# Kernel tuning notes

Measured on AMD Instinct MI355X. Metric: run time of the kernel, lower is better.

## Reference

```python
import jax, jax.numpy as jnp
import numpy as np

DEPTH = 6
N_EST = 16
IN_DIM = 512
N_CLASSES = 100
BATCH = 8192
N_NODES = 2 ** DEPTH - 1   # 63 internal nodes
N_LEAVES = 2 ** DEPTH      # 64 leaves


def entmax15(t):
    # Source's (nonstandard) entmax15: softmax(relu(t)**1.5)
    z = jax.nn.relu(t)
    return jax.nn.softmax(z ** 1.5, axis=-1)


def _leaf_paths():
    # Ancestor node index and branch bit for every (depth level j, leaf l),
    # exactly matching: idx = 2**(j-1) + l // 2**(depth-(j-1)) - 1
    #                   bit = (l // 2**(depth-j)) % 2
    l = np.arange(N_LEAVES)
    j = np.arange(1, DEPTH + 1)[:, None]
    idx = (2 ** (j - 1) + l[None, :] // (2 ** (DEPTH - (j - 1))) - 1).astype(np.int32)
    bits = ((l[None, :] // (2 ** (DEPTH - j))) % 2).astype(np.int32)
    return jnp.asarray(idx), jnp.asarray(bits)  # both (DEPTH, N_LEAVES)


def setup_inputs() -> dict:
    key = jax.random.key(0)
    kx, kT, kL = jax.random.split(key, 3)
    x = jax.random.normal(kx, (BATCH, IN_DIM), dtype=jnp.float32)
    T = jax.random.normal(kT, (N_EST, N_NODES, IN_DIM), dtype=jnp.float32)
    L = jax.random.normal(kL, (N_EST, N_LEAVES, N_CLASSES), dtype=jnp.float32)
    return {"x": x, "T": T, "L": L}


def reference(x, T, L):
    # Hard feature selection with straight-through: forward = hardmax(entmax15(T)),
    # backward = 0 (in the torch source, I = I - (I - hardmax(I)) kills the gradient).
    I_soft = entmax15(T)  # (E, N, D)
    I = jax.lax.stop_gradient(
        (I_soft == I_soft.max(axis=-1, keepdims=True)).astype(x.dtype)
    )
    # Per-node split decisions for all nodes at once.
    t_dot = jnp.einsum('end,end->en', T, I)          # (E, N) threshold value
    x_dot = jnp.einsum('bd,end->ben', x, I)          # (B, E, N) selected feature
    # s = s - (s - floor(s)) == floor(s); floor has zero gradient (matches torch).
    s = jnp.floor(t_dot[None, :, :] - x_dot)         # (B, E, N)

    idx, bits = _leaf_paths()                        # (DEPTH, N_LEAVES)
    sg = s[..., idx]                                 # (B, E, DEPTH, N_LEAVES)
    factors = jnp.where(bits[None, None] == 1, 1.0 - sg, sg)
    p = jnp.prod(factors, axis=2)                    # (B, E, N_LEAVES)

    # Leaf values, summed over the ensemble.
    y_hat = jnp.einsum('bel,elc->bc', p, L)          # (B, C)
    return jax.nn.softmax(y_hat, axis=-1)
```

## Files before the change

### kernel.cpp

```cpp
#include <hip/hip_runtime.h>
#include <hip/hip_bf16.h>
#include <math.h>

#define IN_DIM 512
#define NC 100
#define NN 63
#define NE 16
#define BATCH 8192
#define XP 516
#define RP 132

typedef __attribute__((ext_vector_type(8))) short bf16x8;
typedef __attribute__((ext_vector_type(4))) float f32x4;

static __device__ __forceinline__ ushort bf16_bits(__hip_bfloat16 h) {
  union { __hip_bfloat16 b; ushort u; } cv; cv.b = h; return cv.u;
}

__global__ __launch_bounds__(256) void prep_kernel(
    const float* __restrict__ T, const float* __restrict__ L,
    ushort* __restrict__ Bfrag, float* __restrict__ tmax, int* __restrict__ dstar) {
  const int tid = threadIdx.x;
  const int bid = blockIdx.x;

  {
    const int i = bid * 256 + tid;
    const int j = i & 7;
    const int lane = (i >> 3) & 63;
    const int cf = (i >> 9) & 7;
    const int hl = (i >> 12) & 1;
    const int kc = i >> 13;
    const int k = kc * 32 + (lane >> 4) * 8 + j;
    const int c = cf * 16 + (lane & 15);
    const float val = (c < NC) ? L[(size_t)k * NC + c] : 0.0f;
    const __hip_bfloat16 hb = __float2bfloat16(val);
    ushort outv;
    if (hl == 0) {
      outv = bf16_bits(hb);
    } else {
      const __hip_bfloat16 lb = __float2bfloat16(val - __bfloat162float(hb));
      outv = bf16_bits(lb);
    }
    Bfrag[i] = outv;
  }

  if (bid < NE * NN && tid < 64) {
    const float4* row = reinterpret_cast<const float4*>(T + (size_t)bid * IN_DIM);
    const int lane = tid;
    float best = -INFINITY;
    int bidx = 0;
#pragma unroll
    for (int i = 0; i < 2; ++i) {
      const int f4 = lane + 64 * i;
      const float4 v = row[f4];
      const int base = f4 * 4;
      if (v.x > best) { best = v.x; bidx = base; }
      if (v.y > best) { best = v.y; bidx = base + 1; }
      if (v.z > best) { best = v.z; bidx = base + 2; }
      if (v.w > best) { best = v.w; bidx = base + 3; }
    }
#pragma unroll
    for (int off = 32; off; off >>= 1) {
      const float ov = __shfl_xor(best, off);
      const int oi = __shfl_xor(bidx, off);
      if (ov > best || (ov == best && oi < bidx)) { best = ov; bidx = oi; }
    }
    if (lane == 0) {
      tmax[bid] = best;
      dstar[bid] = bidx;
    }
  }
}

__global__ __launch_bounds__(512, 2) void forest_fused_kernel(
    const float* __restrict__ x, const ushort* __restrict__ Bfrag,
    const float* __restrict__ tmaxg, const int* __restrict__ dstarg,
    float* __restrict__ out) {
  __shared__ __align__(16) float xl[32 * XP];
  __shared__ __align__(16) int2 tds[NE * 64];
  __shared__ __align__(16) float red[8 * 16 * RP];
  const int tid = threadIdx.x;
  const int b0 = blockIdx.x * 32;
  const int w = tid >> 6, lane = tid & 63;

  {
    const float4* xg = reinterpret_cast<const float4*>(x + (size_t)b0 * IN_DIM);
#pragma unroll
    for (int i = 0; i < 8; ++i) {
      const int idx = tid + i * 512;
      const int r = idx >> 7, c4 = idx & 127;
      *reinterpret_cast<float4*>(&xl[r * XP + c4 * 4]) = xg[r * 128 + c4];
    }
    for (int i = tid; i < NE * NN; i += 512) {
      const int e = (i * 1041) >> 16;
      const int n = i - e * 63;
      tds[e * 64 + 1 + n] = make_int2(dstarg[i], __float_as_int(tmaxg[i]));
    }
  }
  __syncthreads();

  const int r = lane & 15;
  const int lgq = lane >> 4;
  const float* xr0 = &xl[r * XP];
  const float* xr1 = &xl[(r + 16) * XP];
  const bf16x8* bf = reinterpret_cast<const bf16x8*>(Bfrag);

  f32x4 acc0[8], acc1[8];
#pragma unroll
  for (int cf = 0; cf < 8; ++cf) { acc0[cf] = (f32x4)0.0f; acc1[cf] = (f32x4)0.0f; }

  for (int t = 0; t < 4; ++t) {
    const int kc = w * 4 + t;
    const int e = kc >> 1;
    const int lg = (kc & 1) * 4 + lgq;

    const size_t bbase = (size_t)kc * 1024;
    bf16x8 BH[8], BL[8];
#pragma unroll
    for (int cf = 0; cf < 8; ++cf) {
      BH[cf] = bf[bbase + (size_t)cf * 64 + lane];
      BL[cf] = bf[bbase + 512 + (size_t)cf * 64 + lane];
    }

    const int2* tb = &tds[e * 64];
    const int2 T1 = tb[1];
    const int2 T2 = tb[2 + (lg >> 2)];
    const int2 T3 = tb[4 + (lg >> 1)];
    const int2 T4 = tb[8 + lg];
    const int4 P5 = *reinterpret_cast<const int4*>(&tb[16 + 2 * lg]);
    const int4 Q0 = *reinterpret_cast<const int4*>(&tb[32 + 4 * lg]);
    const int4 Q1 = *reinterpret_cast<const int4*>(&tb[34 + 4 * lg]);

    bf16x8 Ah, Al;
    auto agen = [&](const float* xr) {
      const float s1 = floorf(__int_as_float(T1.y) - xr[T1.x]);
      const float s2 = floorf(__int_as_float(T2.y) - xr[T2.x]);
      const float s3 = floorf(__int_as_float(T3.y) - xr[T3.x]);
      const float s4 = floorf(__int_as_float(T4.y) - xr[T4.x]);
      const float s5a = floorf(__int_as_float(P5.y) - xr[P5.x]);
      const float s5b = floorf(__int_as_float(P5.w) - xr[P5.z]);
      const float s60 = floorf(__int_as_float(Q0.y) - xr[Q0.x]);
      const float s61 = floorf(__int_as_float(Q0.w) - xr[Q0.z]);
      const float s62 = floorf(__int_as_float(Q1.y) - xr[Q1.x]);
      const float s63 = floorf(__int_as_float(Q1.w) - xr[Q1.z]);
      const float f1 = ((lg >> 2) & 1) ? 1.0f - s1 : s1;
      const float f2 = ((lg >> 1) & 1) ? 1.0f - s2 : s2;
      const float f3 = (lg & 1) ? 1.0f - s3 : s3;
      const float stem = f1 * f2 * f3;
      const float qa = stem * s4, qb = stem * (1.0f - s4);
      const float w00 = qa * s5a, w01 = qa * (1.0f - s5a);
      const float w10 = qb * s5b, w11 = qb * (1.0f - s5b);
      float p[8];
      p[0] = w00 * s60; p[1] = w00 * (1.0f - s60);
      p[2] = w01 * s61; p[3] = w01 * (1.0f - s61);
      p[4] = w10 * s62; p[5] = w10 * (1.0f - s62);
      p[6] = w11 * s63; p[7] = w11 * (1.0f - s63);
      union { ushort u[8]; bf16x8 v; } H, Lo;
#pragma unroll
      for (int i2 = 0; i2 < 8; ++i2) {
        const __hip_bfloat16 hb = __float2bfloat16(p[i2]);
        const float hf = __bfloat162float(hb);
        H.u[i2] = bf16_bits(hb);
        Lo.u[i2] = bf16_bits(__float2bfloat16(p[i2] - hf));
      }
      Ah = H.v; Al = Lo.v;
    };

    agen(xr0);
#pragma unroll
    for (int cf = 0; cf < 8; ++cf) {
      acc0[cf] = __builtin_amdgcn_mfma_f32_16x16x32_bf16(Ah, BH[cf], acc0[cf], 0, 0, 0);
      acc0[cf] = __builtin_amdgcn_mfma_f32_16x16x32_bf16(Al, BH[cf], acc0[cf], 0, 0, 0);
      acc0[cf] = __builtin_amdgcn_mfma_f32_16x16x32_bf16(Ah, BL[cf], acc0[cf], 0, 0, 0);
      acc0[cf] = __builtin_amdgcn_mfma_f32_16x16x32_bf16(Al, BL[cf], acc0[cf], 0, 0, 0);
    }
    agen(xr1);
#pragma unroll
    for (int cf = 0; cf < 8; ++cf) {
      acc1[cf] = __builtin_amdgcn_mfma_f32_16x16x32_bf16(Ah, BH[cf], acc1[cf], 0, 0, 0);
      acc1[cf] = __builtin_amdgcn_mfma_f32_16x16x32_bf16(Al, BH[cf], acc1[cf], 0, 0, 0);
      acc1[cf] = __builtin_amdgcn_mfma_f32_16x16x32_bf16(Ah, BL[cf], acc1[cf], 0, 0, 0);
      acc1[cf] = __builtin_amdgcn_mfma_f32_16x16x32_bf16(Al, BL[cf], acc1[cf], 0, 0, 0);
    }
  }

  const int rlo = (lane >> 4) * 4;
  const int cl = lane & 15;
  const int rr = tid >> 5;
  const int cg = tid & 31;

  auto epi = [&](const f32x4 (&ac)[8], int rowbase) {
#pragma unroll
    for (int cf = 0; cf < 8; ++cf)
#pragma unroll
      for (int jj = 0; jj < 4; ++jj)
        red[(w * 16 + rlo + jj) * RP + cf * 16 + cl] = ac[cf][jj];
    __syncthreads();
    float v[4] = {0.0f, 0.0f, 0.0f, 0.0f};
#pragma unroll
    for (int pw = 0; pw < 8; ++pw) {
      const float4 rv =
          *reinterpret_cast<const float4*>(&red[(pw * 16 + rr) * RP + cg * 4]);
      v[0] += rv.x; v[1] += rv.y; v[2] += rv.z; v[3] += rv.w;
    }
    float m = -INFINITY;
#pragma unroll
    for (int j = 0; j < 4; ++j)
      if (cg * 4 + j < NC) m = fmaxf(m, v[j]);
#pragma unroll
    for (int off = 1; off < 32; off <<= 1) m = fmaxf(m, __shfl_xor(m, off));
    float ev[4];
    float ss = 0.0f;
#pragma unroll
    for (int j = 0; j < 4; ++j) {
      ev[j] = (cg * 4 + j < NC) ? __expf(v[j] - m) : 0.0f;
      ss += ev[j];
    }
#pragma unroll
    for (int off = 1; off < 32; off <<= 1) ss += __shfl_xor(ss, off);
    const float inv = 1.0f / ss;
    if (cg < 25) {
      float* orow = out + (size_t)(b0 + rowbase + rr) * NC + cg * 4;
      *reinterpret_cast<float4*>(orow) =
          make_float4(ev[0] * inv, ev[1] * inv, ev[2] * inv, ev[3] * inv);
    }
  };

  epi(acc0, 0);
  __syncthreads();
  epi(acc1, 16);
}

extern "C" void kernel_launch(void* const* d_in, const int* in_sizes, int n_in,
                              void* d_out, int out_size, void* d_ws, size_t ws_size,
                              hipStream_t stream) {
  const float* x = (const float*)d_in[0];
  const float* T = (const float*)d_in[1];
  const float* L = (const float*)d_in[2];
  float* out = (float*)d_out;

  char* ws = (char*)d_ws;
  ushort* Bfrag = (ushort*)ws;
  float* tmax = (float*)(ws + 524288);
  int* dstar = (int*)(ws + 528384);

  prep_kernel<<<1024, 256, 0, stream>>>(T, L, Bfrag, tmax, dstar);
  forest_fused_kernel<<<BATCH / 32, 512, 0, stream>>>(x, Bfrag, tmax, dstar, out);
}
```

Baseline: 22.75 us.

## Halve rows per block to 16 and raise occupancy with smaller LDS footprint

Each block now handles 16 batch rows instead of 32, with one accumulator set instead of two. This halves the x tile and reduction buffer in LDS and allows launch bounds of 4 blocks per CU, giving twice as many blocks to spread over the CUs. The epilogue reduces the 8-wave partial sums in two column chunks through a narrower shared buffer, then does a single softmax per row. The cost is that every block must reload the full B fragment set, which doubles that global/L2 traffic for the same batch, and the per-block setup is repeated over more blocks.

New measurement: 24.31 us. 1.07x slower.

```diff
diff --git a/kernel.cpp b/kernel.cpp
--- a/kernel.cpp
+++ b/kernel.cpp
@@ -8,7 +8,7 @@
 #define NE 16
 #define BATCH 8192
 #define XP 516
-#define RP 132
+#define RW 68
 
 typedef __attribute__((ext_vector_type(8))) short bf16x8;
 typedef __attribute__((ext_vector_type(4))) float f32x4;
@@ -72,21 +72,21 @@
   }
 }
 
-__global__ __launch_bounds__(512, 2) void forest_fused_kernel(
+__global__ __launch_bounds__(512, 4) void forest_fused_kernel(
     const float* __restrict__ x, const ushort* __restrict__ Bfrag,
     const float* __restrict__ tmaxg, const int* __restrict__ dstarg,
     float* __restrict__ out) {
-  __shared__ __align__(16) float xl[32 * XP];
+  __shared__ __align__(16) float xl[16 * XP];
   __shared__ __align__(16) int2 tds[NE * 64];
-  __shared__ __align__(16) float red[8 * 16 * RP];
+  __shared__ __align__(16) float red[8 * 16 * RW];
   const int tid = threadIdx.x;
-  const int b0 = blockIdx.x * 32;
+  const int b0 = blockIdx.x * 16;
   const int w = tid >> 6, lane = tid & 63;
 
   {
     const float4* xg = reinterpret_cast<const float4*>(x + (size_t)b0 * IN_DIM);
 #pragma unroll
-    for (int i = 0; i < 8; ++i) {
+    for (int i = 0; i < 4; ++i) {
       const int idx = tid + i * 512;
       const int r = idx >> 7, c4 = idx & 127;
       *reinterpret_cast<float4*>(&xl[r * XP + c4 * 4]) = xg[r * 128 + c4];
@@ -102,13 +102,13 @@
   const int r = lane & 15;
   const int lgq = lane >> 4;
   const float* xr0 = &xl[r * XP];
-  const float* xr1 = &xl[(r + 16) * XP];
   const bf16x8* bf = reinterpret_cast<const bf16x8*>(Bfrag);
 
-  f32x4 acc0[8], acc1[8];
-#pragma unroll
-  for (int cf = 0; cf < 8; ++cf) { acc0[cf] = (f32x4)0.0f; acc1[cf] = (f32x4)0.0f; }
-
+  f32x4 acc[8];
+#pragma unroll
+  for (int cf = 0; cf < 8; ++cf) acc[cf] = (f32x4)0.0f;
+
+#pragma unroll
   for (int t = 0; t < 4; ++t) {
     const int kc = w * 4 + t;
     const int e = kc >> 1;
@@ -131,104 +131,90 @@
     const int4 Q0 = *reinterpret_cast<const int4*>(&tb[32 + 4 * lg]);
     const int4 Q1 = *reinterpret_cast<const int4*>(&tb[34 + 4 * lg]);
 
-    bf16x8 Ah, Al;
-    auto agen = [&](const float* xr) {
-      const float s1 = floorf(__int_as_float(T1.y) - xr[T1.x]);
-      const float s2 = floorf(__int_as_float(T2.y) - xr[T2.x]);
-      const float s3 = floorf(__int_as_float(T3.y) - xr[T3.x]);
-      const float s4 = floorf(__int_as_float(T4.y) - xr[T4.x]);
-      const float s5a = floorf(__int_as_float(P5.y) - xr[P5.x]);
-      const float s5b = floorf(__int_as_float(P5.w) - xr[P5.z]);
-      const float s60 = floorf(__int_as_float(Q0.y) - xr[Q0.x]);
-      const float s61 = floorf(__int_as_float(Q0.w) - xr[Q0.z]);
-      const float s62 = floorf(__int_as_float(Q1.y) - xr[Q1.x]);
-      const float s63 = floorf(__int_as_float(Q1.w) - xr[Q1.z]);
-      const float f1 = ((lg >> 2) & 1) ? 1.0f - s1 : s1;
-      const float f2 = ((lg >> 1) & 1) ? 1.0f - s2 : s2;
-      const float f3 = (lg & 1) ? 1.0f - s3 : s3;
-      const float stem = f1 * f2 * f3;
-      const float qa = stem * s4, qb = stem * (1.0f - s4);
-      const float w00 = qa * s5a, w01 = qa * (1.0f - s5a);
-      const float w10 = qb * s5b, w11 = qb * (1.0f - s5b);
-      float p[8];
-      p[0] = w00 * s60; p[1] = w00 * (1.0f - s60);
-      p[2] = w01 * s61; p[3] = w01 * (1.0f - s61);
-      p[4] = w10 * s62; p[5] = w10 * (1.0f - s62);
-      p[6] = w11 * s63; p[7] = w11 * (1.0f - s63);
-      union { ushort u[8]; bf16x8 v; } H, Lo;
-#pragma unroll
-      for (int i2 = 0; i2 < 8; ++i2) {
-        const __hip_bfloat16 hb = __float2bfloat16(p[i2]);
-        const float hf = __bfloat162float(hb);
-        H.u[i2] = bf16_bits(hb);
-        Lo.u[i2] = bf16_bits(__float2bfloat16(p[i2] - hf));
-      }
-      Ah = H.v; Al = Lo.v;
-    };
-
-    agen(xr0);
+    const float s1 = floorf(__int_as_float(T1.y) - xr0[T1.x]);
+    const float s2 = floorf(__int_as_float(T2.y) - xr0[T2.x]);
+    const float s3 = floorf(__int_as_float(T3.y) - xr0[T3.x]);
+    const float s4 = floorf(__int_as_float(T4.y) - xr0[T4.x]);
+    const float s5a = floorf(__int_as_float(P5.y) - xr0[P5.x]);
+    const float s5b = floorf(__int_as_float(P5.w) - xr0[P5.z]);
+    const float s60 = floorf(__int_as_float(Q0.y) - xr0[Q0.x]);
+    const float s61 = floorf(__int_as_float(Q0.w) - xr0[Q0.z]);
+    const float s62 = floorf(__int_as_float(Q1.y) - xr0[Q1.x]);
+    const float s63 = floorf(__int_as_float(Q1.w) - xr0[Q1.z]);
+    const float f1 = ((lg >> 2) & 1) ? 1.0f - s1 : s1;
+    const float f2 = ((lg >> 1) & 1) ? 1.0f - s2 : s2;
+    const float f3 = (lg & 1) ? 1.0f - s3 : s3;
+    const float stem = f1 * f2 * f3;
+    const float qa = stem * s4, qb = stem * (1.0f - s4);
+    const float w00 = qa * s5a, w01 = qa * (1.0f - s5a);
+    const float w10 = qb * s5b, w11 = qb * (1.0f - s5b);
+    float p[8];
+    p[0] = w00 * s60; p[1] = w00 * (1.0f - s60);
+    p[2] = w01 * s61; p[3] = w01 * (1.0f - s61);
+    p[4] = w10 * s62; p[5] = w10 * (1.0f - s62);
+    p[6] = w11 * s63; p[7] = w11 * (1.0f - s63);
+    union { ushort u[8]; bf16x8 v; } H, Lo;
+#pragma unroll
+    for (int i2 = 0; i2 < 8; ++i2) {
+      const __hip_bfloat16 hb = __float2bfloat16(p[i2]);
+      const float hf = __bfloat162float(hb);
+      H.u[i2] = bf16_bits(hb);
+      Lo.u[i2] = bf16_bits(__float2bfloat16(p[i2] - hf));
+    }
+    const bf16x8 Ah = H.v, Al = Lo.v;
+
 #pragma unroll
     for (int cf = 0; cf < 8; ++cf) {
-      acc0[cf] = __builtin_amdgcn_mfma_f32_16x16x32_bf16(Ah, BH[cf], acc0[cf], 0, 0, 0);
-      acc0[cf] = __builtin_amdgcn_mfma_f32_16x16x32_bf16(Al, BH[cf], acc0[cf], 0, 0, 0);
-      acc0[cf] = __builtin_amdgcn_mfma_f32_16x16x32_bf16(Ah, BL[cf], acc0[cf], 0, 0, 0);
-      acc0[cf] = __builtin_amdgcn_mfma_f32_16x16x32_bf16(Al, BL[cf], acc0[cf], 0, 0, 0);
-    }
-    agen(xr1);
-#pragma unroll
-    for (int cf = 0; cf < 8; ++cf) {
-      acc1[cf] = __builtin_amdgcn_mfma_f32_16x16x32_bf16(Ah, BH[cf], acc1[cf], 0, 0, 0);
-      acc1[cf] = __builtin_amdgcn_mfma_f32_16x16x32_bf16(Al, BH[cf], acc1[cf], 0, 0, 0);
-      acc1[cf] = __builtin_amdgcn_mfma_f32_16x16x32_bf16(Ah, BL[cf], acc1[cf], 0, 0, 0);
-      acc1[cf] = __builtin_amdgcn_mfma_f32_16x16x32_bf16(Al, BL[cf], acc1[cf], 0, 0, 0);
+      acc[cf] = __builtin_amdgcn_mfma_f32_16x16x32_bf16(Ah, BH[cf], acc[cf], 0, 0, 0);
+      acc[cf] = __builtin_amdgcn_mfma_f32_16x16x32_bf16(Al, BH[cf], acc[cf], 0, 0, 0);
+      acc[cf] = __builtin_amdgcn_mfma_f32_16x16x32_bf16(Ah, BL[cf], acc[cf], 0, 0, 0);
+      acc[cf] = __builtin_amdgcn_mfma_f32_16x16x32_bf16(Al, BL[cf], acc[cf], 0, 0, 0);
     }
   }
 
   const int rlo = (lane >> 4) * 4;
   const int cl = lane & 15;
-  const int rr = tid >> 5;
-  const int cg = tid & 31;
-
-  auto epi = [&](const f32x4 (&ac)[8], int rowbase) {
-#pragma unroll
-    for (int cf = 0; cf < 8; ++cf)
+  const int erow = tid >> 5;
+  const int ec = tid & 31;
+
+  float vv[4];
+#pragma unroll
+  for (int ch = 0; ch < 2; ++ch) {
+#pragma unroll
+    for (int cf = 0; cf < 4; ++cf)
 #pragma unroll
       for (int jj = 0; jj < 4; ++jj)
-        red[(w * 16 + rlo + jj) * RP + cf * 16 + cl] = ac[cf][jj];
+        red[(w * 16 + rlo + jj) * RW + cf * 16 + cl] = acc[ch * 4 + cf][jj];
     __syncthreads();
-    float v[4] = {0.0f, 0.0f, 0.0f, 0.0f};
+    float sx = 0.0f, sy = 0.0f;
 #pragma unroll
     for (int pw = 0; pw < 8; ++pw) {
-      const float4 rv =
-          *reinterpret_cast<const float4*>(&red[(pw * 16 + rr) * RP + cg * 4]);
-      v[0] += rv.x; v[1] += rv.y; v[2] += rv.z; v[3] += rv.w;
-    }
-    float m = -INFINITY;
-#pragma unroll
-    for (int j = 0; j < 4; ++j)
-      if (cg * 4 + j < NC) m = fmaxf(m, v[j]);
-#pragma unroll
-    for (int off = 1; off < 32; off <<= 1) m = fmaxf(m, __shfl_xor(m, off));
-    float ev[4];
-    float ss = 0.0f;
-#pragma unroll
-    for (int j = 0; j < 4; ++j) {
-      ev[j] = (cg * 4 + j < NC) ? __expf(v[j] - m) : 0.0f;
-      ss += ev[j];
-    }
-#pragma unroll
-    for (int off = 1; off < 32; off <<= 1) ss += __shfl_xor(ss, off);
-    const float inv = 1.0f / ss;
-    if (cg < 25) {
-      float* orow = out + (size_t)(b0 + rowbase + rr) * NC + cg * 4;
-      *reinterpret_cast<float4*>(orow) =
-          make_float4(ev[0] * inv, ev[1] * inv, ev[2] * inv, ev[3] * inv);
-    }
-  };
-
-  epi(acc0, 0);
-  __syncthreads();
-  epi(acc1, 16);
+      const float2 rv =
+          *reinterpret_cast<const float2*>(&red[(pw * 16 + erow) * RW + ec * 2]);
+      sx += rv.x; sy += rv.y;
+    }
+    vv[ch * 2 + 0] = sx;
+    vv[ch * 2 + 1] = sy;
+    __syncthreads();
+  }
+
+  const int c2 = 64 + ec * 2;
+  float m = fmaxf(vv[0], vv[1]);
+  if (c2 < NC) m = fmaxf(m, fmaxf(vv[2], vv[3]));
+#pragma unroll
+  for (int off = 1; off < 32; off <<= 1) m = fmaxf(m, __shfl_xor(m, off));
+  const float e0 = __expf(vv[0] - m);
+  const float e1 = __expf(vv[1] - m);
+  const float e2 = (c2 < NC) ? __expf(vv[2] - m) : 0.0f;
+  const float e3 = (c2 < NC) ? __expf(vv[3] - m) : 0.0f;
+  float ss = e0 + e1 + e2 + e3;
+#pragma unroll
+  for (int off = 1; off < 32; off <<= 1) ss += __shfl_xor(ss, off);
+  const float inv = 1.0f / ss;
+  float* orow = out + (size_t)(b0 + erow) * NC;
+  *reinterpret_cast<float2*>(orow + ec * 2) = make_float2(e0 * inv, e1 * inv);
+  if (c2 < NC)
+    *reinterpret_cast<float2*>(orow + c2) = make_float2(e2 * inv, e3 * inv);
 }
 
 extern "C" void kernel_launch(void* const* d_in, const int* in_sizes, int n_in,
@@ -245,5 +231,5 @@
   int* dstar = (int*)(ws + 528384);
 
   prep_kernel<<<1024, 256, 0, stream>>>(T, L, Bfrag, tmax, dstar);
-  forest_fused_kernel<<<BATCH / 32, 512, 0, stream>>>(x, Bfrag, tmax, dstar, out);
-}
+  forest_fused_kernel<<<BATCH / 16, 512, 0, stream>>>(x, Bfrag, tmax, dstar, out);
+}
```

## Use 1024-thread blocks with one wave per estimator and chunked epilogue reduction

Applied to the files above, without the earlier changes.

The block grows to 16 waves so each wave handles one estimator (2 k-chunks instead of 4), halving the serial MFMA chain per wave. B fragments are now loaded in pairs inside the MFMA loop instead of all at once, which cuts register pressure enough to allow launch_bounds(1024,4). The epilogue reduces 16 partial tiles in two 64-column chunks through a smaller padded LDS buffer, with one thread per column. The cost is more block-level syncs, a 16-way LDS reduction, and scalar rather than vectorised output stores.

After: 26.44 us. 1.16x slower.

```diff
diff --git a/kernel.cpp b/kernel.cpp
--- a/kernel.cpp
+++ b/kernel.cpp
@@ -8,7 +8,7 @@
 #define NE 16
 #define BATCH 8192
 #define XP 516
-#define RP 132
+#define RW 68
 
 typedef __attribute__((ext_vector_type(8))) short bf16x8;
 typedef __attribute__((ext_vector_type(4))) float f32x4;
@@ -72,13 +72,13 @@
   }
 }
 
-__global__ __launch_bounds__(512, 2) void forest_fused_kernel(
+__global__ __launch_bounds__(1024, 4) void forest_fused_kernel(
     const float* __restrict__ x, const ushort* __restrict__ Bfrag,
     const float* __restrict__ tmaxg, const int* __restrict__ dstarg,
     float* __restrict__ out) {
   __shared__ __align__(16) float xl[32 * XP];
   __shared__ __align__(16) int2 tds[NE * 64];
-  __shared__ __align__(16) float red[8 * 16 * RP];
+  __shared__ __align__(16) float red[16 * 16 * RW];
   const int tid = threadIdx.x;
   const int b0 = blockIdx.x * 32;
   const int w = tid >> 6, lane = tid & 63;
@@ -86,12 +86,12 @@
   {
     const float4* xg = reinterpret_cast<const float4*>(x + (size_t)b0 * IN_DIM);
 #pragma unroll
-    for (int i = 0; i < 8; ++i) {
-      const int idx = tid + i * 512;
+    for (int i = 0; i < 4; ++i) {
+      const int idx = tid + i * 1024;
       const int r = idx >> 7, c4 = idx & 127;
       *reinterpret_cast<float4*>(&xl[r * XP + c4 * 4]) = xg[r * 128 + c4];
     }
-    for (int i = tid; i < NE * NN; i += 512) {
+    for (int i = tid; i < NE * NN; i += 1024) {
       const int e = (i * 1041) >> 16;
       const int n = i - e * 63;
       tds[e * 64 + 1 + n] = make_int2(dstarg[i], __float_as_int(tmaxg[i]));
@@ -109,18 +109,11 @@
 #pragma unroll
   for (int cf = 0; cf < 8; ++cf) { acc0[cf] = (f32x4)0.0f; acc1[cf] = (f32x4)0.0f; }
 
-  for (int t = 0; t < 4; ++t) {
-    const int kc = w * 4 + t;
-    const int e = kc >> 1;
-    const int lg = (kc & 1) * 4 + lgq;
-
+  for (int t = 0; t < 2; ++t) {
+    const int kc = w * 2 + t;
+    const int e = w;
+    const int lg = t * 4 + lgq;
     const size_t bbase = (size_t)kc * 1024;
-    bf16x8 BH[8], BL[8];
-#pragma unroll
-    for (int cf = 0; cf < 8; ++cf) {
-      BH[cf] = bf[bbase + (size_t)cf * 64 + lane];
-      BL[cf] = bf[bbase + 512 + (size_t)cf * 64 + lane];
-    }
 
     const int2* tb = &tds[e * 64];
     const int2 T1 = tb[1];
@@ -131,8 +124,8 @@
     const int4 Q0 = *reinterpret_cast<const int4*>(&tb[32 + 4 * lg]);
     const int4 Q1 = *reinterpret_cast<const int4*>(&tb[34 + 4 * lg]);
 
-    bf16x8 Ah, Al;
-    auto agen = [&](const float* xr) {
+    bf16x8 Ah0, Al0, Ah1, Al1;
+    auto agen = [&](const float* xr, bf16x8& Ah, bf16x8& Al) {
       const float s1 = floorf(__int_as_float(T1.y) - xr[T1.x]);
       const float s2 = floorf(__int_as_float(T2.y) - xr[T2.x]);
       const float s3 = floorf(__int_as_float(T3.y) - xr[T3.x]);
@@ -165,70 +158,73 @@
       }
       Ah = H.v; Al = Lo.v;
     };
-
-    agen(xr0);
-#pragma unroll
-    for (int cf = 0; cf < 8; ++cf) {
-      acc0[cf] = __builtin_amdgcn_mfma_f32_16x16x32_bf16(Ah, BH[cf], acc0[cf], 0, 0, 0);
-      acc0[cf] = __builtin_amdgcn_mfma_f32_16x16x32_bf16(Al, BH[cf], acc0[cf], 0, 0, 0);
-      acc0[cf] = __builtin_amdgcn_mfma_f32_16x16x32_bf16(Ah, BL[cf], acc0[cf], 0, 0, 0);
-      acc0[cf] = __builtin_amdgcn_mfma_f32_16x16x32_bf16(Al, BL[cf], acc0[cf], 0, 0, 0);
-    }
-    agen(xr1);
-#pragma unroll
-    for (int cf = 0; cf < 8; ++cf) {
-      acc1[cf] = __builtin_amdgcn_mfma_f32_16x16x32_bf16(Ah, BH[cf], acc1[cf], 0, 0, 0);
-      acc1[cf] = __builtin_amdgcn_mfma_f32_16x16x32_bf16(Al, BH[cf], acc1[cf], 0, 0, 0);
-      acc1[cf] = __builtin_amdgcn_mfma_f32_16x16x32_bf16(Ah, BL[cf], acc1[cf], 0, 0, 0);
-      acc1[cf] = __builtin_amdgcn_mfma_f32_16x16x32_bf16(Al, BL[cf], acc1[cf], 0, 0, 0);
+    agen(xr0, Ah0, Al0);
+    agen(xr1, Ah1, Al1);
+
+#pragma unroll
+    for (int bc = 0; bc < 4; ++bc) {
+      const int cf0 = bc * 2;
+      bf16x8 BH0 = bf[bbase + (size_t)cf0 * 64 + lane];
+      bf16x8 BL0 = bf[bbase + 512 + (size_t)cf0 * 64 + lane];
+      bf16x8 BH1 = bf[bbase + (size_t)(cf0 + 1) * 64 + lane];
+      bf16x8 BL1 = bf[bbase + 512 + (size_t)(cf0 + 1) * 64 + lane];
+      acc0[cf0] = __builtin_amdgcn_mfma_f32_16x16x32_bf16(Ah0, BH0, acc0[cf0], 0, 0, 0);
+      acc0[cf0] = __builtin_amdgcn_mfma_f32_16x16x32_bf16(Al0, BH0, acc0[cf0], 0, 0, 0);
+      acc0[cf0] = __builtin_amdgcn_mfma_f32_16x16x32_bf16(Ah0, BL0, acc0[cf0], 0, 0, 0);
+      acc0[cf0] = __builtin_amdgcn_mfma_f32_16x16x32_bf16(Al0, BL0, acc0[cf0], 0, 0, 0);
+      acc1[cf0] = __builtin_amdgcn_mfma_f32_16x16x32_bf16(Ah1, BH0, acc1[cf0], 0, 0, 0);
+      acc1[cf0] = __builtin_amdgcn_mfma_f32_16x16x32_bf16(Al1, BH0, acc1[cf0], 0, 0, 0);
+      acc1[cf0] = __builtin_amdgcn_mfma_f32_16x16x32_bf16(Ah1, BL0, acc1[cf0], 0, 0, 0);
+      acc1[cf0] = __builtin_amdgcn_mfma_f32_16x16x32_bf16(Al1, BL0, acc1[cf0], 0, 0, 0);
+      acc0[cf0 + 1] = __builtin_amdgcn_mfma_f32_16x16x32_bf16(Ah0, BH1, acc0[cf0 + 1], 0, 0, 0);
+      acc0[cf0 + 1] = __builtin_amdgcn_mfma_f32_16x16x32_bf16(Al0, BH1, acc0[cf0 + 1], 0, 0, 0);
+      acc0[cf0 + 1] = __builtin_amdgcn_mfma_f32_16x16x32_bf16(Ah0, BL1, acc0[cf0 + 1], 0, 0, 0);
+      acc0[cf0 + 1] = __builtin_amdgcn_mfma_f32_16x16x32_bf16(Al0, BL1, acc0[cf0 + 1], 0, 0, 0);
+      acc1[cf0 + 1] = __builtin_amdgcn_mfma_f32_16x16x32_bf16(Ah1, BH1, acc1[cf0 + 1], 0, 0, 0);
+      acc1[cf0 + 1] = __builtin_amdgcn_mfma_f32_16x16x32_bf16(Al1, BH1, acc1[cf0 + 1], 0, 0, 0);
+      acc1[cf0 + 1] = __builtin_amdgcn_mfma_f32_16x16x32_bf16(Ah1, BL1, acc1[cf0 + 1], 0, 0, 0);
+      acc1[cf0 + 1] = __builtin_amdgcn_mfma_f32_16x16x32_bf16(Al1, BL1, acc1[cf0 + 1], 0, 0, 0);
     }
   }
 
   const int rlo = (lane >> 4) * 4;
   const int cl = lane & 15;
-  const int rr = tid >> 5;
-  const int cg = tid & 31;
-
-  auto epi = [&](const f32x4 (&ac)[8], int rowbase) {
-#pragma unroll
-    for (int cf = 0; cf < 8; ++cf)
-#pragma unroll
-      for (int jj = 0; jj < 4; ++jj)
-        red[(w * 16 + rlo + jj) * RP + cf * 16 + cl] = ac[cf][jj];
-    __syncthreads();
-    float v[4] = {0.0f, 0.0f, 0.0f, 0.0f};
-#pragma unroll
-    for (int pw = 0; pw < 8; ++pw) {
-      const float4 rv =
-          *reinterpret_cast<const float4*>(&red[(pw * 16 + rr) * RP + cg * 4]);
-      v[0] += rv.x; v[1] += rv.y; v[2] += rv.z; v[3] += rv.w;
-    }
-    float m = -INFINITY;
-#pragma unroll
-    for (int j = 0; j < 4; ++j)
-      if (cg * 4 + j < NC) m = fmaxf(m, v[j]);
-#pragma unroll
-    for (int off = 1; off < 32; off <<= 1) m = fmaxf(m, __shfl_xor(m, off));
-    float ev[4];
-    float ss = 0.0f;
-#pragma unroll
-    for (int j = 0; j < 4; ++j) {
-      ev[j] = (cg * 4 + j < NC) ? __expf(v[j] - m) : 0.0f;
-      ss += ev[j];
-    }
-#pragma unroll
-    for (int off = 1; off < 32; off <<= 1) ss += __shfl_xor(ss, off);
+  const int erow = w;
+  const int ec = lane;
+
+#pragma unroll
+  for (int tile = 0; tile < 2; ++tile) {
+    float vlo = 0.0f, vhi = 0.0f;
+#pragma unroll
+    for (int ch = 0; ch < 2; ++ch) {
+#pragma unroll
+      for (int cf4 = 0; cf4 < 4; ++cf4) {
+        const f32x4 a = tile ? acc1[ch * 4 + cf4] : acc0[ch * 4 + cf4];
+#pragma unroll
+        for (int jj = 0; jj < 4; ++jj)
+          red[(w * 16 + rlo + jj) * RW + cf4 * 16 + cl] = a[jj];
+      }
+      __syncthreads();
+      float s = 0.0f;
+#pragma unroll
+      for (int p = 0; p < 16; ++p) s += red[(p * 16 + erow) * RW + ec];
+      if (ch == 0) vlo = s; else vhi = s;
+      __syncthreads();
+    }
+    const float v2 = (ec + 64 < NC) ? vhi : -INFINITY;
+    float m = fmaxf(vlo, v2);
+#pragma unroll
+    for (int off = 32; off; off >>= 1) m = fmaxf(m, __shfl_xor(m, off));
+    const float e1 = __expf(vlo - m);
+    const float e2 = (ec + 64 < NC) ? __expf(vhi - m) : 0.0f;
+    float ss = e1 + e2;
+#pragma unroll
+    for (int off = 32; off; off >>= 1) ss += __shfl_xor(ss, off);
     const float inv = 1.0f / ss;
-    if (cg < 25) {
-      float* orow = out + (size_t)(b0 + rowbase + rr) * NC + cg * 4;
-      *reinterpret_cast<float4*>(orow) =
-          make_float4(ev[0] * inv, ev[1] * inv, ev[2] * inv, ev[3] * inv);
-    }
-  };
-
-  epi(acc0, 0);
-  __syncthreads();
-  epi(acc1, 16);
+    float* orow = out + (size_t)(b0 + tile * 16 + erow) * NC;
+    orow[ec] = e1 * inv;
+    if (ec + 64 < NC) orow[ec + 64] = e2 * inv;
+  }
 }
 
 extern "C" void kernel_launch(void* const* d_in, const int* in_sizes, int n_in,
@@ -245,5 +241,5 @@
   int* dstar = (int*)(ws + 528384);
 
   prep_kernel<<<1024, 256, 0, stream>>>(T, L, Bfrag, tmax, dstar);
-  forest_fused_kernel<<<BATCH / 32, 512, 0, stream>>>(x, Bfrag, tmax, dstar, out);
-}
+  forest_fused_kernel<<<BATCH / 32, 1024, 0, stream>>>(x, Bfrag, tmax, dstar, out);
+}
```
